# Optimization experiments

Hardware: AMD Instinct MI355X
Metric: run time of the kernel (lower is better)

## Reference

```python
import jax, jax.numpy as jnp
import numpy as np

HID = 128
NEG = 9000000000000000.0  # 9e15 additive mask constant from the source


def setup_inputs() -> dict:
    key = jax.random.key(0)
    ks = jax.random.split(key, 20)
    B, N, OBS, N1, N2 = 32, 2048, 256, 8, 8
    x = jax.random.normal(ks[0], (B, N, OBS), dtype=jnp.float32)
    mask = jax.random.randint(ks[1], (B, N, N), 0, 2).astype(jnp.float32)

    def lin(kw, kb, fan_in, fan_out):
        bound = 1.0 / np.sqrt(fan_in)
        W = jax.random.uniform(kw, (fan_in, fan_out), jnp.float32, -bound, bound)
        b = jax.random.uniform(kb, (fan_out,), jnp.float32, -bound, bound)
        return W, b

    Wv, bv = lin(ks[2], ks[3], OBS, HID)
    Wk, bk = lin(ks[4], ks[5], OBS, HID)
    Wq, bq = lin(ks[6], ks[7], OBS, HID)
    Wout, bout = lin(ks[8], ks[9], HID, HID)
    Wval, bval = lin(ks[10], ks[11], HID, 1)
    Wadv1, badv1 = lin(ks[12], ks[13], HID, N1)
    Wadv2, badv2 = lin(ks[14], ks[15], HID, N2)
    return {
        'x': x, 'mask': mask,
        'Wv': Wv, 'bv': bv, 'Wk': Wk, 'bk': bk, 'Wq': Wq, 'bq': bq,
        'Wout': Wout, 'bout': bout, 'Wval': Wval, 'bval': bval,
        'Wadv1': Wadv1, 'badv1': badv1, 'Wadv2': Wadv2, 'badv2': badv2,
    }


def reference(x, mask, Wv, bv, Wk, bk, Wq, bq, Wout, bout,
              Wval, bval, Wadv1, badv1, Wadv2, badv2):
    # AttenModel
    v = jax.nn.relu(x @ Wv + bv)          # [B,N,H]
    q = jax.nn.relu(x @ Wq + bq)          # [B,N,H]
    k = jax.nn.relu(x @ Wk + bk)          # [B,N,H]
    scores = jnp.einsum('bnh,bmh->bnm', q, k)          # [B,N,N]
    scores = scores * mask - NEG * (1.0 - mask)
    att = jax.nn.softmax(scores, axis=2)
    out = jnp.einsum('bnm,bmh->bnh', att, v)            # [B,N,H]
    out = jax.nn.relu(out @ Wout + bout)                # [B,N,H]
    # Dueling heads (batch > 1, so squeeze(0) is a no-op)
    value = out @ Wval + bval                            # [B,N,1]
    adv1 = out @ Wadv1 + badv1                           # [B,N,n1]
    adv2 = out @ Wadv2 + badv2                           # [B,N,n2]
    q1 = value + adv1 - adv1.mean(axis=1, keepdims=True)
    q2 = value + adv2 - adv2.mean(axis=1, keepdims=True)
    return (q1, q2)
```

## Files before the change

### kernel.cpp

```cpp
#include <hip/hip_runtime.h>
#include <hip/hip_bf16.h>


typedef __attribute__((ext_vector_type(4))) float f32x4;
typedef __attribute__((ext_vector_type(8))) short bf16x8;
typedef __attribute__((ext_vector_type(4))) unsigned int u32x4;

#define LOG2E 1.44269504088896340736f
#define NEGC 9.0e15f

static __device__ __forceinline__ unsigned short f2bf(float f) {
  unsigned int x = __builtin_bit_cast(unsigned int, f);
  unsigned int r = (x + 0x7fffu + ((x >> 16) & 1u)) >> 16;
  return (unsigned short)r;
}
static __device__ __forceinline__ float bf2f(unsigned short u) {
  return __builtin_bit_cast(float, ((unsigned int)u) << 16);
}
static __device__ __forceinline__ unsigned int pack2bf(float lo, float hi) {
  return (unsigned int)f2bf(lo) | ((unsigned int)f2bf(hi) << 16);
}
static __device__ __forceinline__ f32x4 mfma16(bf16x8 a, bf16x8 b, f32x4 c) {
  return __builtin_amdgcn_mfma_f32_16x16x32_bf16(a, b, c, 0, 0, 0);
}

__global__ __launch_bounds__(256) void prepack_kernel(const float* __restrict__ mask,
                                                      unsigned long long* __restrict__ bits) {
  const int lane = threadIdx.x & 63;
  const int gwave = (blockIdx.x << 2) | (threadIdx.x >> 6);
  const int T = lane & 3;
  const int sh = T << 4;
  for (int r = 0; r < 8; ++r) {
    const long row = (long)gwave * 8 + r;
    const float* mp = mask + row * 2048;
    unsigned long long* op = bits + row * 32;
#pragma unroll
    for (int g = 0; g < 8; ++g) {
      f32x4 v = *(const f32x4*)(mp + g * 256 + lane * 4);
      unsigned long long b0 = __ballot(v[0] != 0.0f);
      unsigned long long b1 = __ballot(v[1] != 0.0f);
      unsigned long long b2 = __ballot(v[2] != 0.0f);
      unsigned long long b3 = __ballot(v[3] != 0.0f);
      unsigned long long f0 = (b0 >> sh) & 0xFFFFull;
      unsigned long long f1 = (b1 >> sh) & 0xFFFFull;
      unsigned long long f2 = (b2 >> sh) & 0xFFFFull;
      unsigned long long f3 = (b3 >> sh) & 0xFFFFull;
      unsigned long long val = f0 | (f1 << 16) | (f2 << 32) | (f3 << 48);
      if (lane < 4) op[g * 4 + T] = val;
    }
  }
}

__global__ __launch_bounds__(256) void prep_kernel(
    const float* __restrict__ Wv, const float* __restrict__ Wk,
    const float* __restrict__ Wq, const float* __restrict__ Wout,
    unsigned short* __restrict__ Wf_hi, unsigned short* __restrict__ Wf_lo,
    unsigned short* __restrict__ WoutT) {
  int gid = blockIdx.x * 256 + threadIdx.x;
  if (gid < 12288) {
    int kc = gid / 1536;
    int rem = gid - kc * 1536;
    int t = rem >> 6, lane = rem & 63;
    int hf = lane & 15, qf = lane >> 4;
    int sec = t >> 3;
    int j = (t & 7) * 16 + hf;
    const float* W = (sec == 0) ? Wq : (sec == 1) ? Wk : Wv;
#pragma unroll
    for (int e = 0; e < 8; ++e) {
      int k = kc * 32 + qf * 8 + e;
      float w = W[k * 128 + j];
      unsigned short hi = f2bf(w);
      Wf_hi[gid * 8 + e] = hi;
      Wf_lo[gid * 8 + e] = f2bf(w - bf2f(hi));
    }
  } else if (gid < 12288 + 16384) {
    int i2 = gid - 12288;
    int j = i2 >> 7, c = i2 & 127;
    WoutT[i2] = f2bf(Wout[c * 128 + j]);
  }
}

__global__ __launch_bounds__(512, 2) void proj_kernel(
    const float* __restrict__ x,
    const unsigned short* __restrict__ Wf_hi, const unsigned short* __restrict__ Wf_lo,
    const float* __restrict__ bq, const float* __restrict__ bk, const float* __restrict__ bv,
    unsigned short* __restrict__ q_bf, unsigned short* __restrict__ Kf,
    unsigned short* __restrict__ Vf) {
  __shared__ bf16x8 wst_hi[1536];
  __shared__ bf16x8 wst_lo[1536];
  __shared__ unsigned short vbuf[128][136];

  const int tid = threadIdx.x;
  const int lane = tid & 63, wid = tid >> 6;
  const int qq = lane >> 4, hh = lane & 15;
  const long rbase = (long)blockIdx.x * 128;
  const long rowA = rbase + wid * 16 + hh;
  const f32x4 zero4 = {0.f, 0.f, 0.f, 0.f};
  f32x4 acc[24];
#pragma unroll
  for (int t = 0; t < 24; ++t) acc[t] = zero4;

  for (int kc = 0; kc < 8; ++kc) {
    __syncthreads();
#pragma unroll
    for (int i = 0; i < 3; ++i) {
      int idx = i * 512 + tid;
      wst_hi[idx] = *(const bf16x8*)(Wf_hi + ((long)kc * 1536 + idx) * 8);
      wst_lo[idx] = *(const bf16x8*)(Wf_lo + ((long)kc * 1536 + idx) * 8);
    }
    __syncthreads();

    const float* xp = x + rowA * 256 + kc * 32 + qq * 8;
    f32x4 x0 = *(const f32x4*)xp;
    f32x4 x1 = *(const f32x4*)(xp + 4);
    bf16x8 ah, al;
#pragma unroll
    for (int j = 0; j < 8; ++j) {
      float f = (j < 4) ? x0[j] : x1[j - 4];
      unsigned short h = f2bf(f);
      ah[j] = (short)h;
      al[j] = (short)f2bf(f - bf2f(h));
    }
#pragma unroll
    for (int t = 0; t < 24; ++t) {
      bf16x8 bh = wst_hi[t * 64 + lane];
      bf16x8 bl = wst_lo[t * 64 + lane];
      acc[t] = mfma16(ah, bh, acc[t]);
      acc[t] = mfma16(al, bh, acc[t]);
      acc[t] = mfma16(ah, bl, acc[t]);
    }
  }

  const int rowL = wid * 16 + qq * 4;
  const int b = (int)(rbase >> 11);
  const int tbase = (int)((rbase & 2047) >> 6);

  for (int sec = 0; sec < 3; ++sec) {
    __syncthreads();
#pragma unroll
    for (int tp = 0; tp < 8; ++tp) {
      const int t = sec * 8 + tp;
      const int j = tp * 16 + hh;
      const float bias = (sec == 0) ? bq[j] : (sec == 1) ? bk[j] : bv[j];
#pragma unroll
      for (int r = 0; r < 4; ++r) {
        unsigned short h = f2bf(fmaxf(acc[t][r] + bias, 0.f));
        if (sec == 2) vbuf[j][rowL + r] = h;
        else          vbuf[rowL + r][j] = h;
      }
    }
    __syncthreads();
    if (sec == 0) {
      const int row = tid >> 2, ch = tid & 3;
      bf16x8 w = *(const bf16x8*)&vbuf[row][ch * 32];
      bf16x8 w2 = *(const bf16x8*)&vbuf[row][ch * 32 + 8];
      bf16x8 w3 = *(const bf16x8*)&vbuf[row][ch * 32 + 16];
      bf16x8 w4 = *(const bf16x8*)&vbuf[row][ch * 32 + 24];
      unsigned short* op = q_bf + (rbase + row) * 128 + ch * 32;
      *(bf16x8*)op = w; *(bf16x8*)(op + 8) = w2;
      *(bf16x8*)(op + 16) = w3; *(bf16x8*)(op + 24) = w4;
    } else if (sec == 1) {
#pragma unroll
      for (int it = 0; it < 4; ++it) {
        int gid = it * 512 + tid;
        int tt = gid >> 10, m = (gid >> 8) & 3, kc = (gid >> 6) & 3, ln = gid & 63;
        int hf = ln & 15, qf = ln >> 4;
        bf16x8 w = *(const bf16x8*)&vbuf[tt * 64 + m * 16 + hf][kc * 32 + qf * 8];
        long off = (((long)(b * 32 + tbase + tt) * 16 + m * 4 + kc) * 64 + ln) * 8;
        *(bf16x8*)(Kf + off) = w;
      }
    } else {
#pragma unroll
      for (int it = 0; it < 4; ++it) {
        int gid = it * 512 + tid;
        int tt = gid >> 10, ht = (gid >> 7) & 7, c = (gid >> 6) & 1, ln = gid & 63;
        int hf = ln & 15, qf = ln >> 4;
        bf16x8 w = *(const bf16x8*)&vbuf[ht * 16 + hf][tt * 64 + c * 32 + qf * 8];
        long off = (((long)(b * 32 + tbase + tt) * 16 + ht * 2 + c) * 64 + ln) * 8;
        *(bf16x8*)(Vf + off) = w;
      }
    }
  }
}

__global__ __launch_bounds__(256, 2) void attn_kernel(
    const unsigned short* __restrict__ q_bf, const unsigned short* __restrict__ Kf,
    const unsigned short* __restrict__ Vf,
    const unsigned long long* __restrict__ bits, unsigned short* __restrict__ out_att) {
  __shared__ bf16x8 kls[2][1024];
  __shared__ bf16x8 vls[2][1024];

  const int tid = threadIdx.x;
  const int lane = tid & 63, wid = tid >> 6;
  const int qq = lane >> 4, hh = lane & 15;
  const int orig = blockIdx.x;
  const int b = ((orig & 7) << 2) | ((orig >> 3) & 3);
  const int nb = orig >> 5;
  const long qbase = (long)b * 2048 + nb * 128 + wid * 32;

  const f32x4 zero4 = {0.f, 0.f, 0.f, 0.f};

  bf16x8 qh[2][4];
#pragma unroll
  for (int ctq = 0; ctq < 2; ++ctq)
#pragma unroll
    for (int kc = 0; kc < 4; ++kc)
      qh[ctq][kc] = *(const bf16x8*)(q_bf + (qbase + ctq * 16 + hh) * 128 + kc * 32 + qq * 8);

  const unsigned long long* br0 = bits + (qbase + hh) * 32;
  const unsigned long long* br1 = bits + (qbase + 16 + hh) * 32;
  const unsigned short* kf0 = Kf + (long)(b * 32) * 8192;
  const unsigned short* vf0 = Vf + (long)(b * 32) * 8192;

  f32x4 o_acc[8][2];
#pragma unroll
  for (int ht = 0; ht < 8; ++ht) { o_acc[ht][0] = zero4; o_acc[ht][1] = zero4; }
  float m_run[2] = {-3.0e38f, -3.0e38f};
  float l_run[2] = {0.f, 0.f};

  bf16x8 stg[8];
  const int seg0 = wid * 8;
  auto LOADREG = [&](int t) {
#pragma unroll
    for (int i = 0; i < 8; ++i) {
      int seg = seg0 + i;
      const unsigned short* src = (seg < 16)
          ? kf0 + (long)t * 8192 + (seg * 64 + lane) * 8
          : vf0 + (long)t * 8192 + ((seg - 16) * 64 + lane) * 8;
      stg[i] = *(const bf16x8*)src;
    }
  };
  auto WRITEBUF = [&](int nb2) {
#pragma unroll
    for (int i = 0; i < 8; ++i) {
      int seg = seg0 + i;
      if (seg < 16) kls[nb2][seg * 64 + lane] = stg[i];
      else          vls[nb2][(seg - 16) * 64 + lane] = stg[i];
    }
  };

  LOADREG(0);
  WRITEBUF(0);
  LOADREG(1);
  __syncthreads();

  unsigned long long bc0 = br0[0];
  unsigned long long bc1 = br1[0];

  const int src0 = (((qq << 1)) & 3) * 16 + hh;
  const int src1 = (((qq << 1) + 1) & 3) * 16 + hh;
  const bool hiq = qq >= 2;
  int cur = 0;

  for (int t = 0; t < 32; ++t) {
    unsigned long long bn0 = 0, bn1 = 0;
    if (t + 1 < 32) { bn0 = br0[t + 1]; bn1 = br1[t + 1]; }

    if (t + 1 < 32) WRITEBUF(cur ^ 1);
    if (t + 2 < 32) LOADREG(t + 2);

    f32x4 s[2][4];
#pragma unroll
    for (int m = 0; m < 4; ++m) { s[0][m] = zero4; s[1][m] = zero4; }
    __builtin_amdgcn_s_setprio(1);
#pragma unroll
    for (int m = 0; m < 4; ++m) {
      bf16x8 khf[4];
#pragma unroll
      for (int kc = 0; kc < 4; ++kc) khf[kc] = kls[cur][(m * 4 + kc) * 64 + lane];
#pragma unroll
      for (int kc = 0; kc < 4; ++kc)
#pragma unroll
        for (int ctq = 0; ctq < 2; ++ctq)
          s[ctq][m] = mfma16(khf[kc], qh[ctq][kc], s[ctq][m]);
    }
    __builtin_amdgcn_s_setprio(0);

    {
      const unsigned long long bb0 = bc0 >> qq;
      const unsigned long long bb1 = bc1 >> qq;
#pragma unroll
      for (int m = 0; m < 4; ++m)
#pragma unroll
        for (int r = 0; r < 4; ++r) {
          const int sh = r * 16 + m * 4;
          s[0][m][r] = ((bb0 >> sh) & 1ull) ? s[0][m][r] : -NEGC;
          s[1][m][r] = ((bb1 >> sh) & 1ull) ? s[1][m][r] : -NEGC;
        }
    }

    unsigned int pk[2][4][2];
#pragma unroll
    for (int ctq = 0; ctq < 2; ++ctq) {
      float mx = s[ctq][0][0];
#pragma unroll
      for (int m = 0; m < 4; ++m)
#pragma unroll
        for (int r = 0; r < 4; ++r) mx = fmaxf(mx, s[ctq][m][r]);
      mx = fmaxf(mx, __shfl_xor(mx, 16, 64));
      mx = fmaxf(mx, __shfl_xor(mx, 32, 64));
      if (__any(mx > m_run[ctq] + 8.0f)) {
        float mnew = fmaxf(m_run[ctq], mx);
        float sc = exp2f((m_run[ctq] - mnew) * LOG2E);
        m_run[ctq] = mnew;
        l_run[ctq] *= sc;
#pragma unroll
        for (int ht = 0; ht < 8; ++ht) o_acc[ht][ctq] *= sc;
      }
      float ps = 0.f;
#pragma unroll
      for (int m = 0; m < 4; ++m)
#pragma unroll
        for (int r = 0; r < 4; ++r) {
          float p = exp2f((s[ctq][m][r] - m_run[ctq]) * LOG2E);
          s[ctq][m][r] = p;
          ps += p;
        }
      ps += __shfl_xor(ps, 16, 64);
      ps += __shfl_xor(ps, 32, 64);
      l_run[ctq] += ps;
#pragma unroll
      for (int m = 0; m < 4; ++m) {
        pk[ctq][m][0] = pack2bf(s[ctq][m][0], s[ctq][m][1]);
        pk[ctq][m][1] = pack2bf(s[ctq][m][2], s[ctq][m][3]);
      }
    }

    bf16x8 pb[2][2];
#pragma unroll
    for (int ctq = 0; ctq < 2; ++ctq)
#pragma unroll
      for (int c = 0; c < 2; ++c) {
        unsigned int a0 = (unsigned int)__shfl((int)pk[ctq][2 * c][0], src0, 64);
        unsigned int a1 = (unsigned int)__shfl((int)pk[ctq][2 * c][1], src0, 64);
        unsigned int a2 = (unsigned int)__shfl((int)pk[ctq][2 * c][0], src1, 64);
        unsigned int a3 = (unsigned int)__shfl((int)pk[ctq][2 * c][1], src1, 64);
        unsigned int b0 = (unsigned int)__shfl((int)pk[ctq][2 * c + 1][0], src0, 64);
        unsigned int b1 = (unsigned int)__shfl((int)pk[ctq][2 * c + 1][1], src0, 64);
        unsigned int b2 = (unsigned int)__shfl((int)pk[ctq][2 * c + 1][0], src1, 64);
        unsigned int b3 = (unsigned int)__shfl((int)pk[ctq][2 * c + 1][1], src1, 64);
        u32x4 w;
        w[0] = hiq ? b0 : a0;
        w[1] = hiq ? b1 : a1;
        w[2] = hiq ? b2 : a2;
        w[3] = hiq ? b3 : a3;
        pb[ctq][c] = __builtin_bit_cast(bf16x8, w);
      }

    __builtin_amdgcn_s_setprio(1);
#pragma unroll
    for (int ht = 0; ht < 8; ++ht)
#pragma unroll
      for (int c = 0; c < 2; ++c) {
        bf16x8 vf = vls[cur][(ht * 2 + c) * 64 + lane];
#pragma unroll
        for (int ctq = 0; ctq < 2; ++ctq)
          o_acc[ht][ctq] = mfma16(vf, pb[ctq][c], o_acc[ht][ctq]);
      }
    __builtin_amdgcn_s_setprio(0);

    __syncthreads();
    cur ^= 1;
    bc0 = bn0;
    bc1 = bn1;
  }

#pragma unroll
  for (int ctq = 0; ctq < 2; ++ctq) {
    float inv = 1.0f / l_run[ctq];
    const long row = qbase + ctq * 16 + hh;
#pragma unroll
    for (int ht = 0; ht < 8; ++ht) {
      f32x4 o = o_acc[ht][ctq];
      uint2 w;
      w.x = pack2bf(o[0] * inv, o[1] * inv);
      w.y = pack2bf(o[2] * inv, o[3] * inv);
      *(uint2*)(out_att + row * 128 + ht * 16 + qq * 4) = w;
    }
  }
}

__global__ __launch_bounds__(256) void wout_heads_kernel(
    const unsigned short* __restrict__ out_att, const unsigned short* __restrict__ WoutT,
    const float* __restrict__ bout,
    const float* __restrict__ Wval, const float* __restrict__ bval,
    const float* __restrict__ Wadv1, const float* __restrict__ badv1,
    const float* __restrict__ Wadv2, const float* __restrict__ badv2,
    float* __restrict__ value, float* __restrict__ adv1, float* __restrict__ adv2) {
  const int lane = threadIdx.x & 63, wid = threadIdx.x >> 6;
  const int qq = lane >> 4, hh = lane & 15;
  const long rowA = (long)blockIdx.x * 64 + wid * 16 + hh;
  const f32x4 zero4 = {0.f, 0.f, 0.f, 0.f};
  f32x4 acc[8];
#pragma unroll
  for (int t = 0; t < 8; ++t) acc[t] = zero4;
#pragma unroll
  for (int kc = 0; kc < 4; ++kc) {
    bf16x8 af = *(const bf16x8*)(out_att + rowA * 128 + kc * 32 + qq * 8);
#pragma unroll
    for (int t = 0; t < 8; ++t) {
      bf16x8 bf = *(const bf16x8*)(WoutT + (t * 16 + hh) * 128 + kc * 32 + qq * 8);
      acc[t] = mfma16(af, bf, acc[t]);
    }
  }
  float pv[4] = {0.f, 0.f, 0.f, 0.f};
  float pa1[4][8], pa2[4][8];
#pragma unroll
  for (int r = 0; r < 4; ++r)
#pragma unroll
    for (int j = 0; j < 8; ++j) { pa1[r][j] = 0.f; pa2[r][j] = 0.f; }
#pragma unroll
  for (int t = 0; t < 8; ++t) {
    const int col = t * 16 + hh;
    const float bo = bout[col];
    const float wv = Wval[col];
    const f32x4 w1a = *(const f32x4*)(Wadv1 + col * 8);
    const f32x4 w1b = *(const f32x4*)(Wadv1 + col * 8 + 4);
    const f32x4 w2a = *(const f32x4*)(Wadv2 + col * 8);
    const f32x4 w2b = *(const f32x4*)(Wadv2 + col * 8 + 4);
#pragma unroll
    for (int r = 0; r < 4; ++r) {
      float h = fmaxf(acc[t][r] + bo, 0.f);
      pv[r] += h * wv;
#pragma unroll
      for (int j = 0; j < 4; ++j) {
        pa1[r][j]     += h * w1a[j];
        pa1[r][4 + j] += h * w1b[j];
        pa2[r][j]     += h * w2a[j];
        pa2[r][4 + j] += h * w2b[j];
      }
    }
  }
#pragma unroll
  for (int r = 0; r < 4; ++r) {
#pragma unroll
    for (int s = 1; s < 16; s <<= 1) {
      pv[r] += __shfl_xor(pv[r], s, 64);
#pragma unroll
      for (int j = 0; j < 8; ++j) {
        pa1[r][j] += __shfl_xor(pa1[r][j], s, 64);
        pa2[r][j] += __shfl_xor(pa2[r][j], s, 64);
      }
    }
  }
  if (hh == 0) {
    const float bv0 = bval[0];
#pragma unroll
    for (int r = 0; r < 4; ++r) {
      const long row = (long)blockIdx.x * 64 + wid * 16 + qq * 4 + r;
      value[row] = pv[r] + bv0;
#pragma unroll
      for (int j = 0; j < 8; ++j) {
        adv1[row * 8 + j] = pa1[r][j] + badv1[j];
        adv2[row * 8 + j] = pa2[r][j] + badv2[j];
      }
    }
  }
}

__global__ __launch_bounds__(256) void sums_kernel(const float* __restrict__ adv1,
                                                   const float* __restrict__ adv2,
                                                   float* __restrict__ sums) {
  const int b = blockIdx.x, tid = threadIdx.x;
  __shared__ float red[4][16];
  float p[16];
#pragma unroll
  for (int j = 0; j < 16; ++j) p[j] = 0.f;
  for (int n = tid; n < 2048; n += 256) {
    const long row = (long)b * 2048 + n;
    const f32x4 a1a = *(const f32x4*)(adv1 + row * 8);
    const f32x4 a1b = *(const f32x4*)(adv1 + row * 8 + 4);
    const f32x4 a2a = *(const f32x4*)(adv2 + row * 8);
    const f32x4 a2b = *(const f32x4*)(adv2 + row * 8 + 4);
#pragma unroll
    for (int j = 0; j < 4; ++j) {
      p[j] += a1a[j]; p[4 + j] += a1b[j];
      p[8 + j] += a2a[j]; p[12 + j] += a2b[j];
    }
  }
#pragma unroll
  for (int s = 1; s < 64; s <<= 1)
#pragma unroll
    for (int j = 0; j < 16; ++j) p[j] += __shfl_xor(p[j], s, 64);
  const int wid = tid >> 6;
  if ((tid & 63) == 0)
#pragma unroll
    for (int j = 0; j < 16; ++j) red[wid][j] = p[j];
  __syncthreads();
  if (tid < 16)
    sums[b * 16 + tid] = red[0][tid] + red[1][tid] + red[2][tid] + red[3][tid];
}

__global__ void combine_kernel(const float* __restrict__ value, const float* __restrict__ adv1,
                               const float* __restrict__ adv2, const float* __restrict__ sums,
                               float* __restrict__ out) {
  const int idx = blockIdx.x * 256 + threadIdx.x;
  const int half = 524288;
  const int which = (idx >= half) ? 1 : 0;
  const int rem = idx - which * half;
  const int b = rem >> 14;
  const int r2 = rem & 16383;
  const int n = r2 >> 3, j = r2 & 7;
  const long row = (long)b * 2048 + n;
  const float* adv = which ? adv2 : adv1;
  const float mean = sums[b * 16 + which * 8 + j] * (1.0f / 2048.0f);
  out[idx] = value[row] + adv[row * 8 + j] - mean;
}

extern "C" void kernel_launch(void* const* d_in, const int* in_sizes, int n_in,
                              void* d_out, int out_size, void* d_ws, size_t ws_size,
                              hipStream_t stream) {
  const float* x     = (const float*)d_in[0];
  const float* mask  = (const float*)d_in[1];
  const float* Wv    = (const float*)d_in[2];
  const float* bv    = (const float*)d_in[3];
  const float* Wk    = (const float*)d_in[4];
  const float* bk    = (const float*)d_in[5];
  const float* Wq    = (const float*)d_in[6];
  const float* bq    = (const float*)d_in[7];
  const float* Wout  = (const float*)d_in[8];
  const float* bout  = (const float*)d_in[9];
  const float* Wval  = (const float*)d_in[10];
  const float* bval  = (const float*)d_in[11];
  const float* Wadv1 = (const float*)d_in[12];
  const float* badv1 = (const float*)d_in[13];
  const float* Wadv2 = (const float*)d_in[14];
  const float* badv2 = (const float*)d_in[15];
  float* out = (float*)d_out;
  char* ws = (char*)d_ws;

  unsigned short* q_bf   = (unsigned short*)(ws + 0);
  unsigned short* Kf     = (unsigned short*)(ws + 16777216);
  unsigned short* Vf     = (unsigned short*)(ws + 33554432);
  unsigned short* out_at = (unsigned short*)(ws + 50331648);
  float* value = (float*)(ws + 67108864);
  float* adv1  = (float*)(ws + 67371008);
  float* adv2  = (float*)(ws + 69468160);
  float* sums  = (float*)(ws + 71565312);
  unsigned short* Wf_hi = (unsigned short*)(ws + 71567360);
  unsigned short* Wf_lo = (unsigned short*)(ws + 71763968);
  unsigned short* WoutT = (unsigned short*)(ws + 71960576);
  unsigned long long* bits = (unsigned long long*)(ws + 71993344);

  prepack_kernel<<<2048, 256, 0, stream>>>(mask, bits);
  prep_kernel<<<112, 256, 0, stream>>>(Wv, Wk, Wq, Wout, Wf_hi, Wf_lo, WoutT);
  proj_kernel<<<512, 512, 0, stream>>>(x, Wf_hi, Wf_lo, bq, bk, bv, q_bf, Kf, Vf);
  attn_kernel<<<512, 256, 0, stream>>>(q_bf, Kf, Vf, bits, out_at);
  wout_heads_kernel<<<1024, 256, 0, stream>>>(out_at, WoutT, bout, Wval, bval,
                                              Wadv1, badv1, Wadv2, badv2,
                                              value, adv1, adv2);
  sums_kernel<<<32, 256, 0, stream>>>(adv1, adv2, sums);
  combine_kernel<<<4096, 256, 0, stream>>>(value, adv1, adv2, sums, out);
}
```

Before: 348.9 us.

## Fuse mask bit-packing into projection kernel with interleaved block roles

Merges the mask prepack kernel and the QKV projection kernel into one launch, where every third block does projection and the other two pack mask bits. Projection blocks shrink from 128 rows and 512 threads to 64 rows and 256 threads, with the LDS staging buffer resized to match. The aim is to overlap the bandwidth-bound mask read with the MFMA-bound projection and to drop a launch. The cost is that each projection block now reloads the full weight tiles for half as many rows, doubling weight staging traffic.

```diff
diff --git a/kernel.cpp b/kernel.cpp
--- a/kernel.cpp
+++ b/kernel.cpp
@@ -22,33 +22,6 @@
 }
 static __device__ __forceinline__ f32x4 mfma16(bf16x8 a, bf16x8 b, f32x4 c) {
   return __builtin_amdgcn_mfma_f32_16x16x32_bf16(a, b, c, 0, 0, 0);
-}
-
-__global__ __launch_bounds__(256) void prepack_kernel(const float* __restrict__ mask,
-                                                      unsigned long long* __restrict__ bits) {
-  const int lane = threadIdx.x & 63;
-  const int gwave = (blockIdx.x << 2) | (threadIdx.x >> 6);
-  const int T = lane & 3;
-  const int sh = T << 4;
-  for (int r = 0; r < 8; ++r) {
-    const long row = (long)gwave * 8 + r;
-    const float* mp = mask + row * 2048;
-    unsigned long long* op = bits + row * 32;
-#pragma unroll
-    for (int g = 0; g < 8; ++g) {
-      f32x4 v = *(const f32x4*)(mp + g * 256 + lane * 4);
-      unsigned long long b0 = __ballot(v[0] != 0.0f);
-      unsigned long long b1 = __ballot(v[1] != 0.0f);
-      unsigned long long b2 = __ballot(v[2] != 0.0f);
-      unsigned long long b3 = __ballot(v[3] != 0.0f);
-      unsigned long long f0 = (b0 >> sh) & 0xFFFFull;
-      unsigned long long f1 = (b1 >> sh) & 0xFFFFull;
-      unsigned long long f2 = (b2 >> sh) & 0xFFFFull;
-      unsigned long long f3 = (b3 >> sh) & 0xFFFFull;
-      unsigned long long val = f0 | (f1 << 16) | (f2 << 32) | (f3 << 48);
-      if (lane < 4) op[g * 4 + T] = val;
-    }
-  }
 }
 
 __global__ __launch_bounds__(256) void prep_kernel(
@@ -80,20 +53,52 @@
   }
 }
 
-__global__ __launch_bounds__(512, 2) void proj_kernel(
+__global__ __launch_bounds__(256, 2) void fused_pp_kernel(
     const float* __restrict__ x,
     const unsigned short* __restrict__ Wf_hi, const unsigned short* __restrict__ Wf_lo,
     const float* __restrict__ bq, const float* __restrict__ bk, const float* __restrict__ bv,
     unsigned short* __restrict__ q_bf, unsigned short* __restrict__ Kf,
-    unsigned short* __restrict__ Vf) {
+    unsigned short* __restrict__ Vf,
+    const float* __restrict__ mask, unsigned long long* __restrict__ bits) {
   __shared__ bf16x8 wst_hi[1536];
   __shared__ bf16x8 wst_lo[1536];
-  __shared__ unsigned short vbuf[128][136];
+  __shared__ unsigned short vbuf[9216];
 
   const int tid = threadIdx.x;
   const int lane = tid & 63, wid = tid >> 6;
+  const int bid = blockIdx.x;
+  const int role = bid % 3;
+
+  if (role != 0) {
+    const int pidx = (bid / 3) * 2 + (role - 1);
+    const int gwave = pidx * 4 + wid;
+    const int T = lane & 3;
+    const int sh = T << 4;
+    for (int r = 0; r < 8; ++r) {
+      const long row = (long)gwave * 8 + r;
+      const float* mp = mask + row * 2048;
+      unsigned long long* op = bits + row * 32;
+#pragma unroll
+      for (int g = 0; g < 8; ++g) {
+        f32x4 v = *(const f32x4*)(mp + g * 256 + lane * 4);
+        unsigned long long b0 = __ballot(v[0] != 0.0f);
+        unsigned long long b1 = __ballot(v[1] != 0.0f);
+        unsigned long long b2 = __ballot(v[2] != 0.0f);
+        unsigned long long b3 = __ballot(v[3] != 0.0f);
+        unsigned long long f0 = (b0 >> sh) & 0xFFFFull;
+        unsigned long long f1 = (b1 >> sh) & 0xFFFFull;
+        unsigned long long f2 = (b2 >> sh) & 0xFFFFull;
+        unsigned long long f3 = (b3 >> sh) & 0xFFFFull;
+        unsigned long long val = f0 | (f1 << 16) | (f2 << 32) | (f3 << 48);
+        if (lane < 4) op[g * 4 + T] = val;
+      }
+    }
+    return;
+  }
+
+  const int pb = bid / 3;
+  const long rbase = (long)pb * 64;
   const int qq = lane >> 4, hh = lane & 15;
-  const long rbase = (long)blockIdx.x * 128;
   const long rowA = rbase + wid * 16 + hh;
   const f32x4 zero4 = {0.f, 0.f, 0.f, 0.f};
   f32x4 acc[24];
@@ -103,8 +108,8 @@
   for (int kc = 0; kc < 8; ++kc) {
     __syncthreads();
 #pragma unroll
-    for (int i = 0; i < 3; ++i) {
-      int idx = i * 512 + tid;
+    for (int i = 0; i < 6; ++i) {
+      int idx = i * 256 + tid;
       wst_hi[idx] = *(const bf16x8*)(Wf_hi + ((long)kc * 1536 + idx) * 8);
       wst_lo[idx] = *(const bf16x8*)(Wf_lo + ((long)kc * 1536 + idx) * 8);
     }
@@ -145,38 +150,42 @@
 #pragma unroll
       for (int r = 0; r < 4; ++r) {
         unsigned short h = f2bf(fmaxf(acc[t][r] + bias, 0.f));
-        if (sec == 2) vbuf[j][rowL + r] = h;
-        else          vbuf[rowL + r][j] = h;
+        if (sec == 2) vbuf[j * 72 + rowL + r] = h;
+        else          vbuf[(rowL + r) * 136 + j] = h;
       }
     }
     __syncthreads();
     if (sec == 0) {
       const int row = tid >> 2, ch = tid & 3;
-      bf16x8 w = *(const bf16x8*)&vbuf[row][ch * 32];
-      bf16x8 w2 = *(const bf16x8*)&vbuf[row][ch * 32 + 8];
-      bf16x8 w3 = *(const bf16x8*)&vbuf[row][ch * 32 + 16];
-      bf16x8 w4 = *(const bf16x8*)&vbuf[row][ch * 32 + 24];
+      bf16x8 w1 = *(const bf16x8*)&vbuf[row * 136 + ch * 32];
+      bf16x8 w2 = *(const bf16x8*)&vbuf[row * 136 + ch * 32 + 8];
+      bf16x8 w3 = *(const bf16x8*)&vbuf[row * 136 + ch * 32 + 16];
+      bf16x8 w4 = *(const bf16x8*)&vbuf[row * 136 + ch * 32 + 24];
       unsigned short* op = q_bf + (rbase + row) * 128 + ch * 32;
-      *(bf16x8*)op = w; *(bf16x8*)(op + 8) = w2;
-      *(bf16x8*)(op + 16) = w3; *(bf16x8*)(op + 24) = w4;
+      *(bf16x8*)op = w1;
+      *(bf16x8*)(op + 8) = w2;
+      *(bf16x8*)(op + 16) = w3;
+      *(bf16x8*)(op + 24) = w4;
     } else if (sec == 1) {
 #pragma unroll
       for (int it = 0; it < 4; ++it) {
-        int gid = it * 512 + tid;
-        int tt = gid >> 10, m = (gid >> 8) & 3, kc = (gid >> 6) & 3, ln = gid & 63;
+        int gid = it * 256 + tid;
+        int seg = gid >> 6, ln = gid & 63;
+        int m = seg >> 2, kc = seg & 3;
         int hf = ln & 15, qf = ln >> 4;
-        bf16x8 w = *(const bf16x8*)&vbuf[tt * 64 + m * 16 + hf][kc * 32 + qf * 8];
-        long off = (((long)(b * 32 + tbase + tt) * 16 + m * 4 + kc) * 64 + ln) * 8;
+        bf16x8 w = *(const bf16x8*)&vbuf[(m * 16 + hf) * 136 + kc * 32 + qf * 8];
+        long off = (((long)(b * 32 + tbase) * 16 + seg) * 64 + ln) * 8;
         *(bf16x8*)(Kf + off) = w;
       }
     } else {
 #pragma unroll
       for (int it = 0; it < 4; ++it) {
-        int gid = it * 512 + tid;
-        int tt = gid >> 10, ht = (gid >> 7) & 7, c = (gid >> 6) & 1, ln = gid & 63;
+        int gid = it * 256 + tid;
+        int seg = gid >> 6, ln = gid & 63;
+        int ht = seg >> 1, c = seg & 1;
         int hf = ln & 15, qf = ln >> 4;
-        bf16x8 w = *(const bf16x8*)&vbuf[ht * 16 + hf][tt * 64 + c * 32 + qf * 8];
-        long off = (((long)(b * 32 + tbase + tt) * 16 + ht * 2 + c) * 64 + ln) * 8;
+        bf16x8 w = *(const bf16x8*)&vbuf[(ht * 16 + hf) * 72 + c * 32 + qf * 8];
+        long off = (((long)(b * 32 + tbase) * 16 + seg) * 64 + ln) * 8;
         *(bf16x8*)(Vf + off) = w;
       }
     }
@@ -542,9 +551,9 @@
   unsigned short* WoutT = (unsigned short*)(ws + 71960576);
   unsigned long long* bits = (unsigned long long*)(ws + 71993344);
 
-  prepack_kernel<<<2048, 256, 0, stream>>>(mask, bits);
   prep_kernel<<<112, 256, 0, stream>>>(Wv, Wk, Wq, Wout, Wf_hi, Wf_lo, WoutT);
-  proj_kernel<<<512, 512, 0, stream>>>(x, Wf_hi, Wf_lo, bq, bk, bv, q_bf, Kf, Vf);
+  fused_pp_kernel<<<3072, 256, 0, stream>>>(x, Wf_hi, Wf_lo, bq, bk, bv,
+                                            q_bf, Kf, Vf, mask, bits);
   attn_kernel<<<512, 256, 0, stream>>>(q_bf, Kf, Vf, bits, out_at);
   wout_heads_kernel<<<1024, 256, 0, stream>>>(out_at, WoutT, bout, Wval, bval,
                                               Wadv1, badv1, Wadv2, badv2,
```

New measurement: 400.6 us. +14.8%, slower.
